# Performance work log

Hardware: AMD Instinct MI355X
Metric: run time of the kernel (lower is better)

## Reference

```python
import jax, jax.numpy as jnp
import numpy as np

N, D, M = 100000, 128, 2048


def setup_inputs() -> dict:
    key = jax.random.key(0)
    k1, k2, k3, k4 = jax.random.split(key, 4)
    X = jax.random.normal(k1, (N, D), dtype=jnp.float32)
    Y = jax.random.normal(k2, (N, 1), dtype=jnp.float32)
    centers = jax.random.normal(k3, (M, D), dtype=jnp.float32)
    # alpha is a buffer produced by an inner Falkon solve; use small random values
    alpha = jax.random.normal(k4, (M, 1), dtype=jnp.float32) * 0.01
    sigma = jnp.asarray(1.0, dtype=jnp.float32)     # Gaussian kernel lengthscale (nn.Parameter)
    penalty = jnp.asarray(5.0, dtype=jnp.float32)   # lambda = exp(-penalty)
    return {"X": X, "Y": Y, "centers": centers, "alpha": alpha,
            "sigma": sigma, "penalty": penalty}


def _rbf_mmv(A, B, v, sigma):
    # Gaussian (RBF) kernel mat-vec: exp(-||a-b||^2 / (2 sigma^2)) @ v
    # A:[n,d], B:[m,d], v:[m,1] -> [n,1]
    a2 = jnp.sum(A * A, axis=-1, keepdims=True)          # [n,1]
    b2 = jnp.sum(B * B, axis=-1, keepdims=True).T        # [1,m]
    sq = a2 + b2 - 2.0 * (A @ B.T)                       # [n,m] squared distances
    Kmat = jnp.exp(-sq / (2.0 * sigma * sigma))
    return Kmat @ v


def reference(X, Y, centers, alpha, sigma, penalty):
    # loss = mean((K_NM @ alpha - Y)^2) + exp(-penalty) * alpha^T K_MM alpha
    preds = _rbf_mmv(X, centers, alpha, sigma)                     # [N,1]
    loss = jnp.mean((preds - Y) ** 2)
    pen = jnp.exp(-penalty)
    reg = pen * (alpha.T @ _rbf_mmv(centers, centers, alpha, sigma))  # [1,1]
    total = loss + reg[0, 0]
    return total, preds
```

## Files before the change

kernel.cpp:

```cpp
#include <hip/hip_runtime.h>
#include <stdint.h>

typedef short short8 __attribute__((ext_vector_type(8)));
typedef float f32x4 __attribute__((ext_vector_type(4)));

__device__ __forceinline__ unsigned short f32_to_bf16(float f) {
    uint32_t u = __builtin_bit_cast(uint32_t, f);
    u += 0x7FFFu + ((u >> 16) & 1u);
    return (unsigned short)(u >> 16);
}
__device__ __forceinline__ float bf16_to_f32(unsigned short h) {
    return __builtin_bit_cast(float, (uint32_t)h << 16);
}

__global__ void prep_kernel(const float* __restrict__ C,
                            const float* __restrict__ alpha,
                            const float* __restrict__ sigma,
                            unsigned short* __restrict__ Bp,
                            float2* __restrict__ cw,
                            float* __restrict__ acc)
{
    const int t = threadIdx.x;
    const int g = blockIdx.x;
    const int r = t >> 4;
    const int c16 = t & 15;
    const int R = g * 16 + r;

    if (g == 0 && t == 0) {
        acc[0] = 0.f; acc[1] = 0.f;
        ((unsigned int*)acc)[2] = 0u;
    }

    const float4* src = (const float4*)(C + (size_t)R * 128 + c16 * 8);
    float4 va = src[0], vb = src[1];
    unsigned short h[8];
    h[0] = f32_to_bf16(va.x); h[1] = f32_to_bf16(va.y);
    h[2] = f32_to_bf16(va.z); h[3] = f32_to_bf16(va.w);
    h[4] = f32_to_bf16(vb.x); h[5] = f32_to_bf16(vb.y);
    h[6] = f32_to_bf16(vb.z); h[7] = f32_to_bf16(vb.w);
    float ss = 0.f;
    #pragma unroll
    for (int k = 0; k < 8; ++k) {
        float f = bf16_to_f32(h[k]);
        ss = fmaf(f, f, ss);
    }
    uint4 pk;
    pk.x = (uint32_t)h[0] | ((uint32_t)h[1] << 16);
    pk.y = (uint32_t)h[2] | ((uint32_t)h[3] << 16);
    pk.z = (uint32_t)h[4] | ((uint32_t)h[5] << 16);
    pk.w = (uint32_t)h[6] | ((uint32_t)h[7] << 16);
    *reinterpret_cast<uint4*>(Bp + (size_t)g * 2048 + c16 * 128 + r * 8) = pk;

    ss += __shfl_xor(ss, 1);
    ss += __shfl_xor(ss, 2);
    ss += __shfl_xor(ss, 4);
    ss += __shfl_xor(ss, 8);
    if (c16 == 0) {
        float sig = sigma[0];
        float q = 0.7213475204444817f / (sig * sig);
        cw[R] = make_float2(ss * q, alpha[R]);
    }
}

__global__ __launch_bounds__(256, 6)
void fused_kernel(const float* __restrict__ X, int N,
                  const float* __restrict__ Yv,
                  const unsigned short* __restrict__ Bp,
                  const float2* __restrict__ cw,
                  const float* __restrict__ alpha,
                  const float* __restrict__ sigma,
                  const float* __restrict__ penalty,
                  int nR, int nMt, int nBlk,
                  float* __restrict__ preds_out,
                  float* __restrict__ out0,
                  float* __restrict__ acc)
{
    __shared__ __align__(16) unsigned short ldsA[8192];
    __shared__ float a2p[64][4];
    __shared__ float predbuf[64][2];

    const int t    = threadIdx.x;
    const int lane = t & 63;
    const int wid  = t >> 6;
    const int h    = wid & 1;
    const int c    = wid >> 1;
    const int l15  = lane & 15;
    const int quad = lane >> 4;

    const float sig = sigma[0];
    const float q  = 0.7213475204444817f / (sig * sig);
    const float q2 = 2.0f * q;

    const bool regmode = (int)blockIdx.x < nR;
    int rowbase;
    float rowterm[2][4];
    short8 a[8];

    if (!regmode) {
        rowbase = ((int)blockIdx.x - nR) * 64;
        const int r_  = t >> 2;
        const int qtr = t & 3;
        const int grow = rowbase + r_;
        unsigned short* dstbase = ldsA + (r_ >> 4) * 2048 + (r_ & 15) * 8;
        float ss = 0.f;
        if (grow < N) {
            const float4* src = (const float4*)(X + (size_t)grow * 128 + qtr * 32);
            #pragma unroll
            for (int cc = 0; cc < 4; ++cc) {
                float4 va = src[2 * cc], vb = src[2 * cc + 1];
                unsigned short h0 = f32_to_bf16(va.x), h1 = f32_to_bf16(va.y);
                unsigned short h2 = f32_to_bf16(va.z), h3 = f32_to_bf16(va.w);
                unsigned short h4 = f32_to_bf16(vb.x), h5 = f32_to_bf16(vb.y);
                unsigned short h6 = f32_to_bf16(vb.z), h7 = f32_to_bf16(vb.w);
                float f0 = bf16_to_f32(h0), f1 = bf16_to_f32(h1);
                float f2 = bf16_to_f32(h2), f3 = bf16_to_f32(h3);
                float f4 = bf16_to_f32(h4), f5 = bf16_to_f32(h5);
                float f6 = bf16_to_f32(h6), f7 = bf16_to_f32(h7);
                ss = fmaf(f0, f0, ss); ss = fmaf(f1, f1, ss);
                ss = fmaf(f2, f2, ss); ss = fmaf(f3, f3, ss);
                ss = fmaf(f4, f4, ss); ss = fmaf(f5, f5, ss);
                ss = fmaf(f6, f6, ss); ss = fmaf(f7, f7, ss);
                uint4 pk;
                pk.x = (uint32_t)h0 | ((uint32_t)h1 << 16);
                pk.y = (uint32_t)h2 | ((uint32_t)h3 << 16);
                pk.z = (uint32_t)h4 | ((uint32_t)h5 << 16);
                pk.w = (uint32_t)h6 | ((uint32_t)h7 << 16);
                *reinterpret_cast<uint4*>(dstbase + (qtr * 4 + cc) * 128) = pk;
            }
        } else {
            uint4 z; z.x = z.y = z.z = z.w = 0u;
            #pragma unroll
            for (int cc = 0; cc < 4; ++cc)
                *reinterpret_cast<uint4*>(dstbase + (qtr * 4 + cc) * 128) = z;
        }
        a2p[r_][qtr] = ss;
        __syncthreads();
        #pragma unroll
        for (int i = 0; i < 2; ++i)
            #pragma unroll
            for (int r = 0; r < 4; ++r) {
                int rl = h * 32 + i * 16 + quad * 4 + r;
                rowterm[i][r] = (a2p[rl][0] + a2p[rl][1] + a2p[rl][2] + a2p[rl][3]) * q;
            }
        const unsigned short* aLds = ldsA + (size_t)(h * 2) * 2048 + lane * 8;
        #pragma unroll
        for (int i = 0; i < 2; ++i)
            #pragma unroll
            for (int kk = 0; kk < 4; ++kk)
                a[i * 4 + kk] = *reinterpret_cast<const short8*>(aLds + (size_t)i * 2048 + kk * 512);
    } else {
        const int b2 = (int)blockIdx.x;
        rowbase = b2 * 64;
        const unsigned short* aG = Bp + (size_t)(b2 * 4 + h * 2) * 2048 + lane * 8;
        #pragma unroll
        for (int i = 0; i < 2; ++i)
            #pragma unroll
            for (int kk = 0; kk < 4; ++kk)
                a[i * 4 + kk] = *reinterpret_cast<const short8*>(aG + (size_t)i * 2048 + kk * 512);
        #pragma unroll
        for (int i = 0; i < 2; ++i)
            #pragma unroll
            for (int r = 0; r < 4; ++r)
                rowterm[i][r] = cw[rowbase + h * 32 + i * 16 + quad * 4 + r].x;
    }

    float srow[2][4] = {};
    const int nG = nMt * 8;
    const int nGper = nG >> 1;
    const int g0 = c * nGper;

    const unsigned short* bBase = Bp + (size_t)g0 * 2048 + lane * 8;
    const float2* cwBase = cw + g0 * 16 + l15;

    for (int s = 0; s < nGper; ++s) {
        const unsigned short* bG = bBase + (size_t)s * 2048;
        short8 b[4];
        #pragma unroll
        for (int kk = 0; kk < 4; ++kk)
            b[kk] = *reinterpret_cast<const short8*>(bG + kk * 512);
        float2 cj = cwBase[s * 16];

        f32x4 acc4[2];
        #pragma unroll
        for (int i = 0; i < 2; ++i) acc4[i] = (f32x4){0.f, 0.f, 0.f, 0.f};
        #pragma unroll
        for (int kk = 0; kk < 4; ++kk)
            #pragma unroll
            for (int i = 0; i < 2; ++i)
                acc4[i] = __builtin_amdgcn_mfma_f32_16x16x32_bf16(
                    a[i * 4 + kk], b[kk], acc4[i], 0, 0, 0);

        #pragma unroll
        for (int i = 0; i < 2; ++i) {
            #pragma unroll
            for (int r = 0; r < 4; ++r) {
                float u = fmaf(acc4[i][r], q2, -(rowterm[i][r] + cj.x));
                float e = __builtin_amdgcn_exp2f(u);
                srow[i][r] = fmaf(e, cj.y, srow[i][r]);
            }
        }
    }

    #pragma unroll
    for (int i = 0; i < 2; ++i) {
        #pragma unroll
        for (int r = 0; r < 4; ++r) {
            int rl = h * 32 + i * 16 + quad * 4 + r;
            float v = srow[i][r];
            v += __shfl_xor(v, 1);
            v += __shfl_xor(v, 2);
            v += __shfl_xor(v, 4);
            v += __shfl_xor(v, 8);
            if (l15 == 0)
                predbuf[rl][c] = v;
        }
    }
    __syncthreads();

    float contrib = 0.f;
    if (t < 64) {
        int grow = rowbase + t;
        if (!regmode) {
            if (grow < N) {
                float pred = predbuf[t][0] + predbuf[t][1];
                preds_out[grow] = pred;
                float d = pred - Yv[grow];
                contrib = d * d;
            }
        } else {
            float pred = predbuf[t][0] + predbuf[t][1];
            contrib = alpha[grow] * pred;
        }
    }
    contrib += __shfl_xor(contrib, 1);
    contrib += __shfl_xor(contrib, 2);
    contrib += __shfl_xor(contrib, 4);
    contrib += __shfl_xor(contrib, 8);
    contrib += __shfl_xor(contrib, 16);
    contrib += __shfl_xor(contrib, 32);
    if (t == 0) atomicAdd(regmode ? (acc + 1) : (acc + 0), contrib);

    __syncthreads();
    if (t == 0) {
        __threadfence();
        unsigned int old = atomicAdd((unsigned int*)(acc + 2), 1u);
        if (old == (unsigned int)(nBlk - 1)) {
            float lv = atomicAdd(acc + 0, 0.0f);
            float rv = atomicAdd(acc + 1, 0.0f);
            out0[0] = lv / (float)N + __expf(-penalty[0]) * rv;
        }
    }
}

extern "C" void kernel_launch(void* const* d_in, const int* in_sizes, int n_in,
                              void* d_out, int out_size, void* d_ws, size_t ws_size,
                              hipStream_t stream) {
    const float* X       = (const float*)d_in[0];
    const float* Y       = (const float*)d_in[1];
    const float* centers = (const float*)d_in[2];
    const float* alpha   = (const float*)d_in[3];
    const float* sigma   = (const float*)d_in[4];
    const float* penalty = (const float*)d_in[5];
    float* out = (float*)d_out;

    const int N = in_sizes[1];
    const int M = in_sizes[3];

    unsigned short* Bp = (unsigned short*)d_ws;
    float2* cw = (float2*)((char*)d_ws + (size_t)M * 256);
    float* acc = (float*)((char*)d_ws + (size_t)M * 264);

    prep_kernel<<<M / 16, 256, 0, stream>>>(centers, alpha, sigma, Bp, cw, acc);

    const int nR  = M / 64;
    const int nA  = (N + 63) / 64;
    const int nMt = M / 128;
    const int nBlk = nR + nA;
    fused_kernel<<<nBlk, 256, 0, stream>>>(X, N, Y, Bp, cw, alpha, sigma, penalty,
                                           nR, nMt, nBlk, out + 1, out, acc);
}
```

Before: 207.4 us.

## Give each wave all 64 rows and split centers four ways across waves

```diff
diff --git a/kernel.cpp b/kernel.cpp
--- a/kernel.cpp
+++ b/kernel.cpp
@@ -3,6 +3,7 @@
 
 typedef short short8 __attribute__((ext_vector_type(8)));
 typedef float f32x4 __attribute__((ext_vector_type(4)));
+typedef float fvec4 __attribute__((ext_vector_type(4)));
 
 __device__ __forceinline__ unsigned short f32_to_bf16(float f) {
     uint32_t u = __builtin_bit_cast(uint32_t, f);
@@ -62,7 +63,7 @@
     }
 }
 
-__global__ __launch_bounds__(256, 6)
+__global__ __launch_bounds__(256, 4)
 void fused_kernel(const float* __restrict__ X, int N,
                   const float* __restrict__ Yv,
                   const unsigned short* __restrict__ Bp,
@@ -77,13 +78,11 @@
 {
     __shared__ __align__(16) unsigned short ldsA[8192];
     __shared__ float a2p[64][4];
-    __shared__ float predbuf[64][2];
+    __shared__ float predbuf[64][4];
 
     const int t    = threadIdx.x;
     const int lane = t & 63;
-    const int wid  = t >> 6;
-    const int h    = wid & 1;
-    const int c    = wid >> 1;
+    const int w    = t >> 6;
     const int l15  = lane & 15;
     const int quad = lane >> 4;
 
@@ -93,8 +92,8 @@
 
     const bool regmode = (int)blockIdx.x < nR;
     int rowbase;
-    float rowterm[2][4];
-    short8 a[8];
+    float rowterm[4][4];
+    short8 a[16];
 
     if (!regmode) {
         rowbase = ((int)blockIdx.x - nR) * 64;
@@ -104,10 +103,11 @@
         unsigned short* dstbase = ldsA + (r_ >> 4) * 2048 + (r_ & 15) * 8;
         float ss = 0.f;
         if (grow < N) {
-            const float4* src = (const float4*)(X + (size_t)grow * 128 + qtr * 32);
+            const fvec4* src = (const fvec4*)(X + (size_t)grow * 128 + qtr * 32);
             #pragma unroll
             for (int cc = 0; cc < 4; ++cc) {
-                float4 va = src[2 * cc], vb = src[2 * cc + 1];
+                fvec4 va = __builtin_nontemporal_load(src + 2 * cc);
+                fvec4 vb = __builtin_nontemporal_load(src + 2 * cc + 1);
                 unsigned short h0 = f32_to_bf16(va.x), h1 = f32_to_bf16(va.y);
                 unsigned short h2 = f32_to_bf16(va.z), h3 = f32_to_bf16(va.w);
                 unsigned short h4 = f32_to_bf16(vb.x), h5 = f32_to_bf16(vb.y);
@@ -136,38 +136,38 @@
         a2p[r_][qtr] = ss;
         __syncthreads();
         #pragma unroll
-        for (int i = 0; i < 2; ++i)
+        for (int i = 0; i < 4; ++i)
             #pragma unroll
             for (int r = 0; r < 4; ++r) {
-                int rl = h * 32 + i * 16 + quad * 4 + r;
+                int rl = i * 16 + quad * 4 + r;
                 rowterm[i][r] = (a2p[rl][0] + a2p[rl][1] + a2p[rl][2] + a2p[rl][3]) * q;
             }
-        const unsigned short* aLds = ldsA + (size_t)(h * 2) * 2048 + lane * 8;
-        #pragma unroll
-        for (int i = 0; i < 2; ++i)
+        const unsigned short* aLds = ldsA + lane * 8;
+        #pragma unroll
+        for (int i = 0; i < 4; ++i)
             #pragma unroll
             for (int kk = 0; kk < 4; ++kk)
                 a[i * 4 + kk] = *reinterpret_cast<const short8*>(aLds + (size_t)i * 2048 + kk * 512);
     } else {
         const int b2 = (int)blockIdx.x;
         rowbase = b2 * 64;
-        const unsigned short* aG = Bp + (size_t)(b2 * 4 + h * 2) * 2048 + lane * 8;
-        #pragma unroll
-        for (int i = 0; i < 2; ++i)
+        const unsigned short* aG = Bp + (size_t)(b2 * 4) * 2048 + lane * 8;
+        #pragma unroll
+        for (int i = 0; i < 4; ++i)
             #pragma unroll
             for (int kk = 0; kk < 4; ++kk)
                 a[i * 4 + kk] = *reinterpret_cast<const short8*>(aG + (size_t)i * 2048 + kk * 512);
         #pragma unroll
-        for (int i = 0; i < 2; ++i)
+        for (int i = 0; i < 4; ++i)
             #pragma unroll
             for (int r = 0; r < 4; ++r)
-                rowterm[i][r] = cw[rowbase + h * 32 + i * 16 + quad * 4 + r].x;
-    }
-
-    float srow[2][4] = {};
+                rowterm[i][r] = cw[rowbase + i * 16 + quad * 4 + r].x;
+    }
+
+    float srow[4][4] = {};
     const int nG = nMt * 8;
-    const int nGper = nG >> 1;
-    const int g0 = c * nGper;
+    const int nGper = nG >> 2;
+    const int g0 = w * nGper;
 
     const unsigned short* bBase = Bp + (size_t)g0 * 2048 + lane * 8;
     const float2* cwBase = cw + g0 * 16 + l15;
@@ -180,18 +180,18 @@
             b[kk] = *reinterpret_cast<const short8*>(bG + kk * 512);
         float2 cj = cwBase[s * 16];
 
-        f32x4 acc4[2];
-        #pragma unroll
-        for (int i = 0; i < 2; ++i) acc4[i] = (f32x4){0.f, 0.f, 0.f, 0.f};
+        f32x4 acc4[4];
+        #pragma unroll
+        for (int i = 0; i < 4; ++i) acc4[i] = (f32x4){0.f, 0.f, 0.f, 0.f};
         #pragma unroll
         for (int kk = 0; kk < 4; ++kk)
             #pragma unroll
-            for (int i = 0; i < 2; ++i)
+            for (int i = 0; i < 4; ++i)
                 acc4[i] = __builtin_amdgcn_mfma_f32_16x16x32_bf16(
                     a[i * 4 + kk], b[kk], acc4[i], 0, 0, 0);
 
         #pragma unroll
-        for (int i = 0; i < 2; ++i) {
+        for (int i = 0; i < 4; ++i) {
             #pragma unroll
             for (int r = 0; r < 4; ++r) {
                 float u = fmaf(acc4[i][r], q2, -(rowterm[i][r] + cj.x));
@@ -202,17 +202,17 @@
     }
 
     #pragma unroll
-    for (int i = 0; i < 2; ++i) {
+    for (int i = 0; i < 4; ++i) {
         #pragma unroll
         for (int r = 0; r < 4; ++r) {
-            int rl = h * 32 + i * 16 + quad * 4 + r;
+            int rl = i * 16 + quad * 4 + r;
             float v = srow[i][r];
             v += __shfl_xor(v, 1);
             v += __shfl_xor(v, 2);
             v += __shfl_xor(v, 4);
             v += __shfl_xor(v, 8);
             if (l15 == 0)
-                predbuf[rl][c] = v;
+                predbuf[rl][w] = v;
         }
     }
     __syncthreads();
@@ -222,13 +222,15 @@
         int grow = rowbase + t;
         if (!regmode) {
             if (grow < N) {
-                float pred = predbuf[t][0] + predbuf[t][1];
+                float pred = (predbuf[t][0] + predbuf[t][1]) +
+                             (predbuf[t][2] + predbuf[t][3]);
                 preds_out[grow] = pred;
                 float d = pred - Yv[grow];
                 contrib = d * d;
             }
         } else {
-            float pred = predbuf[t][0] + predbuf[t][1];
+            float pred = (predbuf[t][0] + predbuf[t][1]) +
+                         (predbuf[t][2] + predbuf[t][3]);
             contrib = alpha[grow] * pred;
         }
     }
```

Measured after the change: 238.3 us. 1.15x slower.
